# Kernel optimization log

Measured on AMD Instinct MI355X. Metric: run time of the kernel, lower is better.

The kernel has to match this reference:

```python
import jax, jax.numpy as jnp
import numpy as np

NUM_CLASSES = 3
LAMBDA_COORD = 5.0
B, A, N = 1048576, 3, 8  # batch, anchors (hardcoded 3 in source), gt boxes per image


def setup_inputs() -> dict:
    key = jax.random.key(0)
    k1, k2, k3 = jax.random.split(key, 3)
    predictions = jax.random.normal(k1, (B, A, 5 + NUM_CLASSES), dtype=jnp.float32)
    gt_boxes = jax.random.uniform(k2, (B, N, 4), dtype=jnp.float32)  # x,y,w,h
    gt_classes = jax.random.randint(k3, (B, N), 0, NUM_CLASSES, dtype=jnp.int32)
    return {"predictions": predictions, "gt_boxes": gt_boxes, "gt_classes": gt_classes}


def reference(predictions, gt_boxes, gt_classes):
    batch = predictions.shape[0]
    # decode predictions, shapes (B, A)
    px = jax.nn.sigmoid(predictions[..., 0])
    py = jax.nn.sigmoid(predictions[..., 1])
    pw = predictions[..., 2]
    ph = predictions[..., 3]
    pconf = jax.nn.sigmoid(predictions[..., 4])
    plogits = predictions[..., 5:]  # (B, A, C)

    # pred corners (B, A, 1)
    px1 = (px - pw / 2)[..., None]; px2 = (px + pw / 2)[..., None]
    py1 = (py - ph / 2)[..., None]; py2 = (py + ph / 2)[..., None]
    # gt corners (B, 1, N)
    gx = gt_boxes[..., 0][:, None, :]; gy = gt_boxes[..., 1][:, None, :]
    gw = gt_boxes[..., 2][:, None, :]; gh = gt_boxes[..., 3][:, None, :]
    gx1 = gx - gw / 2; gx2 = gx + gw / 2
    gy1 = gy - gh / 2; gy2 = gy + gh / 2

    inter_w = jnp.clip(jnp.minimum(px2, gx2) - jnp.maximum(px1, gx1), 0.0)
    inter_h = jnp.clip(jnp.minimum(py2, gy2) - jnp.maximum(py1, gy1), 0.0)
    inter = inter_w * inter_h                              # (B, A, N)
    pred_area = (px2 - px1) * (py2 - py1)                  # (B, A, 1)
    gt_area = (gx2 - gx1) * (gy2 - gy1)                    # (B, 1, N)
    iou = inter / (pred_area + gt_area - inter + 1e-6)     # (B, A, N)

    best_iou = jnp.max(iou, axis=-1)                       # (B, A)
    best_idx = jnp.argmax(iou, axis=-1)                    # (B, A) -- first max, matches strict-> loop
    matched = best_iou > 0.5                               # (B, A)

    mb = jnp.take_along_axis(gt_boxes, best_idx[:, :, None], axis=1)   # (B, A, 4)
    mcls = jnp.take_along_axis(gt_classes, best_idx, axis=1)           # (B, A)

    # coordinate loss: per-scalar mse on matched anchors
    coord = (px - mb[..., 0]) ** 2 + (py - mb[..., 1]) ** 2 \
          + (pw - mb[..., 2]) ** 2 + (ph - mb[..., 3]) ** 2
    coord_loss = jnp.sum(jnp.where(matched, coord, 0.0))

    # confidence BCE, target 1 if matched else 0 (torch BCE clamps log at -100)
    logp = jnp.maximum(jnp.log(pconf), -100.0)
    log1mp = jnp.maximum(jnp.log1p(-pconf), -100.0)
    conf_loss = jnp.sum(jnp.where(matched, -logp, -log1mp))

    # class cross-entropy on matched anchors
    logsm = jax.nn.log_softmax(plogits, axis=-1)                        # (B, A, C)
    nll = -jnp.take_along_axis(logsm, mcls[..., None], axis=-1)[..., 0]  # (B, A)
    class_loss = jnp.sum(jnp.where(matched, nll, 0.0))

    total = LAMBDA_COORD * coord_loss + conf_loss + class_loss
    return total / batch
```

## Files before the change

### kernel.cpp

```cpp
#include <hip/hip_runtime.h>

#define B_SIZE 1048576
#define NBLK   4096
#define NPART  (NBLK * 4)

__device__ __forceinline__ float frcp(float x) { return __builtin_amdgcn_rcpf(x); }

__global__ __launch_bounds__(256) void yolo_loss_kernel(
    const float* __restrict__ pred,
    const float* __restrict__ gt_boxes,
    const int*   __restrict__ gt_classes,
    double* __restrict__ part) {
    __shared__ float4 sBuf[4][64][8];

    const int tid  = threadIdx.x;
    const int wave = tid >> 6;
    const int lane = tid & 63;
    const int wb   = blockIdx.x * 256 + wave * 64;

    const float4* pA = reinterpret_cast<const float4*>(pred     + (size_t)wb * 24);
    const float4* gA = reinterpret_cast<const float4*>(gt_boxes + (size_t)wb * 32);
    float4 vp[6], vg[8];
    #pragma unroll
    for (int k = 0; k < 6; ++k) vp[k] = pA[k * 64 + lane];
    #pragma unroll
    for (int k = 0; k < 8; ++k) vg[k] = gA[k * 64 + lane];
    const int4* cme = reinterpret_cast<const int4*>(gt_classes + (size_t)(wb + lane) * 8);
    const int4 c0 = cme[0], c1 = cme[1];

    float4 (*buf)[8] = sBuf[wave];

    #pragma unroll
    for (int k = 0; k < 6; ++k) {
        const unsigned f  = k * 64 + lane;
        const unsigned bl = f / 6u, of = f % 6u;
        buf[bl][of ^ (bl & 7u)] = vp[k];
    }
    float pr[24];
    #pragma unroll
    for (int s = 0; s < 6; ++s) {
        const float4 t = buf[lane][s ^ (lane & 7)];
        pr[s*4+0] = t.x; pr[s*4+1] = t.y; pr[s*4+2] = t.z; pr[s*4+3] = t.w;
    }

    #pragma unroll
    for (int k = 0; k < 8; ++k) {
        const unsigned f  = k * 64 + lane;
        const unsigned bl = f >> 3, of = f & 7;
        buf[bl][of ^ (bl & 7u)] = vg[k];
    }
    float gb[32];
    #pragma unroll
    for (int s = 0; s < 8; ++s) {
        const float4 t = buf[lane][s ^ (lane & 7)];
        gb[s*4+0] = t.x; gb[s*4+1] = t.y; gb[s*4+2] = t.z; gb[s*4+3] = t.w;
    }
    const int gc[8] = {c0.x, c0.y, c0.z, c0.w, c1.x, c1.y, c1.z, c1.w};

    float total = 0.0f;
    #pragma unroll
    for (int a = 0; a < 3; ++a) {
        const float* p = pr + a * 8;
        const float px = frcp(1.0f + __expf(-p[0]));
        const float py = frcp(1.0f + __expf(-p[1]));
        const float pw = p[2];
        const float ph = p[3];
        const float z  = p[4];
        const float px1 = px - pw * 0.5f, px2 = px + pw * 0.5f;
        const float py1 = py - ph * 0.5f, py2 = py + ph * 0.5f;
        const float pa_eps = (px2 - px1) * (py2 - py1) + 1e-6f;

        float best_iou = -3.4e38f;
        int best_idx = 0;
        #pragma unroll
        for (int n = 0; n < 8; ++n) {
            const float gx = gb[n*4+0], gy = gb[n*4+1];
            const float gw = gb[n*4+2], gh = gb[n*4+3];
            const float hw = gw * 0.5f, hh = gh * 0.5f;
            const float iw = fmaxf(fminf(px2, gx + hw) - fmaxf(px1, gx - hw), 0.0f);
            const float ih = fmaxf(fminf(py2, gy + hh) - fmaxf(py1, gy - hh), 0.0f);
            const float inter = iw * ih;
            const float iou = inter * frcp((pa_eps + gw * gh) - inter);
            const bool upd = iou > best_iou;
            best_iou = upd ? iou : best_iou;
            best_idx = upd ? n : best_idx;
        }
        const bool matched = best_iou > 0.5f;

        float mbx = gb[0], mby = gb[1], mbw = gb[2], mbh = gb[3];
        int mcls = gc[0];
        #pragma unroll
        for (int n = 1; n < 8; ++n) {
            const bool s = (best_idx == n);
            mbx = s ? gb[n*4+0] : mbx;
            mby = s ? gb[n*4+1] : mby;
            mbw = s ? gb[n*4+2] : mbw;
            mbh = s ? gb[n*4+3] : mbh;
            mcls = s ? gc[n] : mcls;
        }

        const float az = fabsf(z);
        const float c  = __logf(1.0f + __expf(-az));
        const float sp_pos = fmaxf(z, 0.0f) + c;
        const float sp_neg = fmaxf(-z, 0.0f) + c;
        total += fminf(matched ? sp_neg : sp_pos, 100.0f);

        if (matched) {
            const float dx = px - mbx, dy = py - mby;
            const float dw = pw - mbw, dh = ph - mbh;
            total += 5.0f * (dx*dx + dy*dy + dw*dw + dh*dh);
            const float l0 = p[5], l1 = p[6], l2 = p[7];
            const float m = fmaxf(l0, fmaxf(l1, l2));
            const float lse = m + __logf(__expf(l0-m) + __expf(l1-m) + __expf(l2-m));
            const float sel = (mcls == 0) ? l0 : ((mcls == 1) ? l1 : l2);
            total += lse - sel;
        }
    }

    #pragma unroll
    for (int off = 32; off > 0; off >>= 1)
        total += __shfl_down(total, off, 64);
    if (lane == 0)
        part[(size_t)blockIdx.x * 4 + wave] = (double)total;
}

__global__ __launch_bounds__(256) void yolo_reduce_kernel(
    const double* __restrict__ part, float* __restrict__ out) {
    double s = 0.0;
    #pragma unroll
    for (int k = 0; k < NPART / 256; ++k)
        s += part[threadIdx.x + k * 256];
    #pragma unroll
    for (int off = 32; off > 0; off >>= 1)
        s += __shfl_down(s, off, 64);
    __shared__ double r[4];
    const int lane = threadIdx.x & 63;
    const int wave = threadIdx.x >> 6;
    if (lane == 0) r[wave] = s;
    __syncthreads();
    if (threadIdx.x == 0)
        out[0] = (float)((r[0] + r[1] + r[2] + r[3]) / (double)B_SIZE);
}

extern "C" void kernel_launch(void* const* d_in, const int* in_sizes, int n_in,
                              void* d_out, int out_size, void* d_ws, size_t ws_size,
                              hipStream_t stream) {
    const float* pred       = (const float*)d_in[0];
    const float* gt_boxes   = (const float*)d_in[1];
    const int*   gt_classes = (const int*)d_in[2];
    float* out   = (float*)d_out;
    double* part = (double*)d_ws;

    yolo_loss_kernel<<<NBLK, 256, 0, stream>>>(pred, gt_boxes, gt_classes, part);
    yolo_reduce_kernel<<<1, 256, 0, stream>>>(part, out);
}
```

Measured before the change: 280.2 us.

## Process four tiles per wave with double-buffered loads, drop LDS transpose

Each wave now handles four batch tiles strided across the grid, loading the next tile into registers while computing the current one, with a quarter as many blocks. It also drops the LDS transpose and has each lane load its own batch element's contiguous 96+128+32 bytes directly. This removes LDS traffic and overlaps memory latency with math, but per-lane loads are strided across lanes, so coalescing is worse and register pressure is higher.

```diff
diff --git a/kernel.cpp b/kernel.cpp
--- a/kernel.cpp
+++ b/kernel.cpp
@@ -1,61 +1,47 @@
 #include <hip/hip_runtime.h>
 
-#define B_SIZE 1048576
-#define NBLK   4096
-#define NPART  (NBLK * 4)
+#define B_SIZE  1048576
+#define NBLK    1024
+#define NWAVE   4096
+#define TILES   4
+#define TSTRIDE (NWAVE * 64)
 
 __device__ __forceinline__ float frcp(float x) { return __builtin_amdgcn_rcpf(x); }
 
-__global__ __launch_bounds__(256) void yolo_loss_kernel(
-    const float* __restrict__ pred,
-    const float* __restrict__ gt_boxes,
-    const int*   __restrict__ gt_classes,
-    double* __restrict__ part) {
-    __shared__ float4 sBuf[4][64][8];
+struct Tile {
+    float4 p[6];
+    float4 g[8];
+    int4   c0, c1;
+};
 
-    const int tid  = threadIdx.x;
-    const int wave = tid >> 6;
-    const int lane = tid & 63;
-    const int wb   = blockIdx.x * 256 + wave * 64;
+__device__ __forceinline__ void tile_load(const float* __restrict__ pred,
+                                          const float* __restrict__ gt_boxes,
+                                          const int*   __restrict__ gt_classes,
+                                          int batch, Tile& t) {
+    const float4* pp = reinterpret_cast<const float4*>(pred       + (size_t)batch * 24);
+    const float4* gp = reinterpret_cast<const float4*>(gt_boxes   + (size_t)batch * 32);
+    const int4*   cp = reinterpret_cast<const int4*>(  gt_classes + (size_t)batch * 8);
+    #pragma unroll
+    for (int k = 0; k < 6; ++k) t.p[k] = pp[k];
+    #pragma unroll
+    for (int k = 0; k < 8; ++k) t.g[k] = gp[k];
+    t.c0 = cp[0]; t.c1 = cp[1];
+}
 
-    const float4* pA = reinterpret_cast<const float4*>(pred     + (size_t)wb * 24);
-    const float4* gA = reinterpret_cast<const float4*>(gt_boxes + (size_t)wb * 32);
-    float4 vp[6], vg[8];
-    #pragma unroll
-    for (int k = 0; k < 6; ++k) vp[k] = pA[k * 64 + lane];
-    #pragma unroll
-    for (int k = 0; k < 8; ++k) vg[k] = gA[k * 64 + lane];
-    const int4* cme = reinterpret_cast<const int4*>(gt_classes + (size_t)(wb + lane) * 8);
-    const int4 c0 = cme[0], c1 = cme[1];
-
-    float4 (*buf)[8] = sBuf[wave];
-
+__device__ __forceinline__ float tile_math(const Tile& t) {
+    float pr[24], gb[32];
     #pragma unroll
     for (int k = 0; k < 6; ++k) {
-        const unsigned f  = k * 64 + lane;
-        const unsigned bl = f / 6u, of = f % 6u;
-        buf[bl][of ^ (bl & 7u)] = vp[k];
+        pr[k*4+0] = t.p[k].x; pr[k*4+1] = t.p[k].y;
+        pr[k*4+2] = t.p[k].z; pr[k*4+3] = t.p[k].w;
     }
-    float pr[24];
-    #pragma unroll
-    for (int s = 0; s < 6; ++s) {
-        const float4 t = buf[lane][s ^ (lane & 7)];
-        pr[s*4+0] = t.x; pr[s*4+1] = t.y; pr[s*4+2] = t.z; pr[s*4+3] = t.w;
-    }
-
     #pragma unroll
     for (int k = 0; k < 8; ++k) {
-        const unsigned f  = k * 64 + lane;
-        const unsigned bl = f >> 3, of = f & 7;
-        buf[bl][of ^ (bl & 7u)] = vg[k];
+        gb[k*4+0] = t.g[k].x; gb[k*4+1] = t.g[k].y;
+        gb[k*4+2] = t.g[k].z; gb[k*4+3] = t.g[k].w;
     }
-    float gb[32];
-    #pragma unroll
-    for (int s = 0; s < 8; ++s) {
-        const float4 t = buf[lane][s ^ (lane & 7)];
-        gb[s*4+0] = t.x; gb[s*4+1] = t.y; gb[s*4+2] = t.z; gb[s*4+3] = t.w;
-    }
-    const int gc[8] = {c0.x, c0.y, c0.z, c0.w, c1.x, c1.y, c1.z, c1.w};
+    const int gc[8] = {t.c0.x, t.c0.y, t.c0.z, t.c0.w,
+                       t.c1.x, t.c1.y, t.c1.z, t.c1.w};
 
     float total = 0.0f;
     #pragma unroll
@@ -116,19 +102,54 @@
             total += lse - sel;
         }
     }
+    return total;
+}
 
+__device__ __forceinline__ float wave_reduce(float v) {
     #pragma unroll
     for (int off = 32; off > 0; off >>= 1)
-        total += __shfl_down(total, off, 64);
+        v += __shfl_down(v, off, 64);
+    return v;
+}
+
+__global__ __launch_bounds__(256) void yolo_loss_kernel(
+    const float* __restrict__ pred,
+    const float* __restrict__ gt_boxes,
+    const int*   __restrict__ gt_classes,
+    double* __restrict__ part) {
+    const int tid  = threadIdx.x;
+    const int wave = tid >> 6;
+    const int lane = tid & 63;
+    const int wid  = blockIdx.x * 4 + wave;
+    const int base = wid * 64 + lane;
+
+    Tile ta, tb;
+    tile_load(pred, gt_boxes, gt_classes, base + 0 * TSTRIDE, ta);
+    tile_load(pred, gt_boxes, gt_classes, base + 1 * TSTRIDE, tb);
+
+    double dacc = 0.0;
+    float  tot;
+
+    tot = tile_math(ta);
+    tile_load(pred, gt_boxes, gt_classes, base + 2 * TSTRIDE, ta);
+    dacc += (double)wave_reduce(tot);
+
+    tot = tile_math(tb);
+    tile_load(pred, gt_boxes, gt_classes, base + 3 * TSTRIDE, tb);
+    dacc += (double)wave_reduce(tot);
+
+    dacc += (double)wave_reduce(tile_math(ta));
+    dacc += (double)wave_reduce(tile_math(tb));
+
     if (lane == 0)
-        part[(size_t)blockIdx.x * 4 + wave] = (double)total;
+        part[wid] = dacc;
 }
 
 __global__ __launch_bounds__(256) void yolo_reduce_kernel(
     const double* __restrict__ part, float* __restrict__ out) {
     double s = 0.0;
     #pragma unroll
-    for (int k = 0; k < NPART / 256; ++k)
+    for (int k = 0; k < NWAVE / 256; ++k)
         s += part[threadIdx.x + k * 256];
     #pragma unroll
     for (int off = 32; off > 0; off >>= 1)
```

Result: no change. 280.5 us (+0.1%).

## Keep per-anchor data in LDS and read lazily to cut register pressure

Applied to the files above, without the earlier changes.

Instead of copying every prediction and gt box from shared memory into register arrays, all data (predictions, boxes, and class ids bit-cast to floats) stays in a wider 16-slot swizzled LDS row per lane. Values are read on demand inside rolled anchor and gt loops, and the matched box and class are fetched by index rather than selected with predicated moves. The goal is fewer VGPRs, so occupancy rises and the memory-bound load phase is hidden better. In exchange the kernel issues more LDS reads, doubles the shared memory per block, and gives up some instruction-level parallelism from the rolled loops.

```diff
diff --git a/kernel.cpp b/kernel.cpp
--- a/kernel.cpp
+++ b/kernel.cpp
@@ -2,7 +2,7 @@
 
 #define B_SIZE 1048576
 #define NBLK   4096
-#define NPART  (NBLK * 4)
+#define NWAVE  (NBLK * 4)
 
 __device__ __forceinline__ float frcp(float x) { return __builtin_amdgcn_rcpf(x); }
 
@@ -11,12 +11,13 @@
     const float* __restrict__ gt_boxes,
     const int*   __restrict__ gt_classes,
     double* __restrict__ part) {
-    __shared__ float4 sBuf[4][64][8];
+    __shared__ float4 sBuf[4][64][16];
 
     const int tid  = threadIdx.x;
     const int wave = tid >> 6;
     const int lane = tid & 63;
-    const int wb   = blockIdx.x * 256 + wave * 64;
+    const int wid  = blockIdx.x * 4 + wave;
+    const int wb   = wid * 64;
 
     const float4* pA = reinterpret_cast<const float4*>(pred     + (size_t)wb * 24);
     const float4* gA = reinterpret_cast<const float4*>(gt_boxes + (size_t)wb * 32);
@@ -28,76 +29,60 @@
     const int4* cme = reinterpret_cast<const int4*>(gt_classes + (size_t)(wb + lane) * 8);
     const int4 c0 = cme[0], c1 = cme[1];
 
-    float4 (*buf)[8] = sBuf[wave];
+    float4 (*buf)[16] = sBuf[wave];
+    const unsigned rx = lane & 15;
 
     #pragma unroll
     for (int k = 0; k < 6; ++k) {
-        const unsigned f  = k * 64 + lane;
-        const unsigned bl = f / 6u, of = f % 6u;
-        buf[bl][of ^ (bl & 7u)] = vp[k];
+        const unsigned f = k * 64 + lane, bl = f / 6u, of = f % 6u;
+        buf[bl][of ^ (bl & 15u)] = vp[k];
     }
-    float pr[24];
-    #pragma unroll
-    for (int s = 0; s < 6; ++s) {
-        const float4 t = buf[lane][s ^ (lane & 7)];
-        pr[s*4+0] = t.x; pr[s*4+1] = t.y; pr[s*4+2] = t.z; pr[s*4+3] = t.w;
-    }
-
     #pragma unroll
     for (int k = 0; k < 8; ++k) {
-        const unsigned f  = k * 64 + lane;
-        const unsigned bl = f >> 3, of = f & 7;
-        buf[bl][of ^ (bl & 7u)] = vg[k];
+        const unsigned f = k * 64 + lane, bl = f >> 3, of = f & 7;
+        buf[bl][(6 + of) ^ (bl & 15u)] = vg[k];
     }
-    float gb[32];
-    #pragma unroll
-    for (int s = 0; s < 8; ++s) {
-        const float4 t = buf[lane][s ^ (lane & 7)];
-        gb[s*4+0] = t.x; gb[s*4+1] = t.y; gb[s*4+2] = t.z; gb[s*4+3] = t.w;
-    }
-    const int gc[8] = {c0.x, c0.y, c0.z, c0.w, c1.x, c1.y, c1.z, c1.w};
+    buf[lane][14 ^ rx] = make_float4(__int_as_float(c0.x), __int_as_float(c0.y),
+                                     __int_as_float(c0.z), __int_as_float(c0.w));
+    buf[lane][15 ^ rx] = make_float4(__int_as_float(c1.x), __int_as_float(c1.y),
+                                     __int_as_float(c1.z), __int_as_float(c1.w));
+
+    const float4* row = buf[lane];
 
     float total = 0.0f;
-    #pragma unroll
+    #pragma unroll 1
     for (int a = 0; a < 3; ++a) {
-        const float* p = pr + a * 8;
-        const float px = frcp(1.0f + __expf(-p[0]));
-        const float py = frcp(1.0f + __expf(-p[1]));
-        const float pw = p[2];
-        const float ph = p[3];
-        const float z  = p[4];
+        const float4 q0 = row[(2 * a)     ^ rx];
+        const float4 q1 = row[(2 * a + 1) ^ rx];
+        const float px = frcp(1.0f + __expf(-q0.x));
+        const float py = frcp(1.0f + __expf(-q0.y));
+        const float pw = q0.z;
+        const float ph = q0.w;
+        const float z  = q1.x;
         const float px1 = px - pw * 0.5f, px2 = px + pw * 0.5f;
         const float py1 = py - ph * 0.5f, py2 = py + ph * 0.5f;
         const float pa_eps = (px2 - px1) * (py2 - py1) + 1e-6f;
 
         float best_iou = -3.4e38f;
         int best_idx = 0;
-        #pragma unroll
+        #pragma unroll 2
         for (int n = 0; n < 8; ++n) {
-            const float gx = gb[n*4+0], gy = gb[n*4+1];
-            const float gw = gb[n*4+2], gh = gb[n*4+3];
-            const float hw = gw * 0.5f, hh = gh * 0.5f;
-            const float iw = fmaxf(fminf(px2, gx + hw) - fmaxf(px1, gx - hw), 0.0f);
-            const float ih = fmaxf(fminf(py2, gy + hh) - fmaxf(py1, gy - hh), 0.0f);
+            const float4 g = row[(6 + n) ^ rx];
+            const float hw = g.z * 0.5f, hh = g.w * 0.5f;
+            const float iw = fmaxf(fminf(px2, g.x + hw) - fmaxf(px1, g.x - hw), 0.0f);
+            const float ih = fmaxf(fminf(py2, g.y + hh) - fmaxf(py1, g.y - hh), 0.0f);
             const float inter = iw * ih;
-            const float iou = inter * frcp((pa_eps + gw * gh) - inter);
+            const float iou = inter * frcp((pa_eps + g.z * g.w) - inter);
             const bool upd = iou > best_iou;
             best_iou = upd ? iou : best_iou;
             best_idx = upd ? n : best_idx;
         }
         const bool matched = best_iou > 0.5f;
 
-        float mbx = gb[0], mby = gb[1], mbw = gb[2], mbh = gb[3];
-        int mcls = gc[0];
-        #pragma unroll
-        for (int n = 1; n < 8; ++n) {
-            const bool s = (best_idx == n);
-            mbx = s ? gb[n*4+0] : mbx;
-            mby = s ? gb[n*4+1] : mby;
-            mbw = s ? gb[n*4+2] : mbw;
-            mbh = s ? gb[n*4+3] : mbh;
-            mcls = s ? gc[n] : mcls;
-        }
+        const float4 mb = row[(6 + best_idx) ^ rx];
+        const float* rowf = reinterpret_cast<const float*>(row);
+        const int cslot = (14 + (best_idx >> 2)) ^ rx;
+        const int mcls  = __float_as_int(rowf[cslot * 4 + (best_idx & 3)]);
 
         const float az = fabsf(z);
         const float c  = __logf(1.0f + __expf(-az));
@@ -106,10 +91,10 @@
         total += fminf(matched ? sp_neg : sp_pos, 100.0f);
 
         if (matched) {
-            const float dx = px - mbx, dy = py - mby;
-            const float dw = pw - mbw, dh = ph - mbh;
+            const float dx = px - mb.x, dy = py - mb.y;
+            const float dw = pw - mb.z, dh = ph - mb.w;
             total += 5.0f * (dx*dx + dy*dy + dw*dw + dh*dh);
-            const float l0 = p[5], l1 = p[6], l2 = p[7];
+            const float l0 = q1.y, l1 = q1.z, l2 = q1.w;
             const float m = fmaxf(l0, fmaxf(l1, l2));
             const float lse = m + __logf(__expf(l0-m) + __expf(l1-m) + __expf(l2-m));
             const float sel = (mcls == 0) ? l0 : ((mcls == 1) ? l1 : l2);
@@ -121,14 +106,14 @@
     for (int off = 32; off > 0; off >>= 1)
         total += __shfl_down(total, off, 64);
     if (lane == 0)
-        part[(size_t)blockIdx.x * 4 + wave] = (double)total;
+        part[wid] = (double)total;
 }
 
 __global__ __launch_bounds__(256) void yolo_reduce_kernel(
     const double* __restrict__ part, float* __restrict__ out) {
     double s = 0.0;
-    #pragma unroll
-    for (int k = 0; k < NPART / 256; ++k)
+    #pragma unroll 8
+    for (int k = 0; k < NWAVE / 256; ++k)
         s += part[threadIdx.x + k * 256];
     #pragma unroll
     for (int off = 32; off > 0; off >>= 1)
```

Result: no change. 278.7 us (-0.5%).
